# Performance work log

Hardware: AMD Instinct MI355X
Metric: run time of the kernel (lower is better)

## Reference

```python
import jax, jax.numpy as jnp
import numpy as np
from jax import lax

IN_PLANES = 512
GROWTH = 32
PLANES = 4 * GROWTH  # 128
EPS = 1e-5


def setup_inputs() -> dict:
    key = jax.random.key(0)
    ks = jax.random.split(key, 10)
    x = jax.random.normal(ks[0], (128, IN_PLANES, 32, 32), dtype=jnp.float32)
    # bn1 affine params (batch-stat BN, track_running_stats=False)
    gamma1 = jax.random.normal(ks[1], (IN_PLANES,), dtype=jnp.float32) * 0.1 + 1.0
    beta1 = jax.random.normal(ks[2], (IN_PLANES,), dtype=jnp.float32) * 0.1
    # convbn1: 1x1 conv weight + folded BN (running stats)
    w1 = jax.random.normal(ks[3], (PLANES, IN_PLANES, 1, 1), dtype=jnp.float32) * (1.0 / np.sqrt(IN_PLANES))
    gamma2 = jax.random.normal(ks[4], (PLANES,), dtype=jnp.float32) * 0.1 + 1.0
    beta2 = jax.random.normal(ks[5], (PLANES,), dtype=jnp.float32) * 0.1
    mean2 = jax.random.normal(ks[6], (PLANES,), dtype=jnp.float32) * 0.1
    var2 = jax.random.uniform(ks[7], (PLANES,), dtype=jnp.float32, minval=0.5, maxval=1.5)
    # conv2: 3x3 conv, padding 1, no bias
    w2 = jax.random.normal(ks[8], (GROWTH, PLANES, 3, 3), dtype=jnp.float32) * (1.0 / np.sqrt(9 * PLANES))
    return {"x": x, "gamma1": gamma1, "beta1": beta1, "w1": w1,
            "gamma2": gamma2, "beta2": beta2, "mean2": mean2, "var2": var2,
            "w2": w2}


def _bn(h, mean, var, gamma, beta):
    # channel-wise affine normalization, NCHW
    inv = lax.rsqrt(var + EPS)
    scale = (gamma * inv)[None, :, None, None]
    shift = (beta - mean * gamma * inv)[None, :, None, None]
    return h * scale + shift


def reference(x, gamma1, beta1, w1, gamma2, beta2, mean2, var2, w2):
    # bn1: batch statistics (track_running_stats=False)
    mu = jnp.mean(x, axis=(0, 2, 3))
    var = jnp.var(x, axis=(0, 2, 3))  # biased, as torch BN normalization
    h = _bn(x, mu, var, gamma1, beta1)
    h = jax.nn.relu(h)
    # convbn1: 1x1 conv then folded BN (running stats)
    h = lax.conv_general_dilated(h, w1, (1, 1), 'VALID',
                                 dimension_numbers=('NCHW', 'OIHW', 'NCHW'))
    h = _bn(h, mean2, var2, gamma2, beta2)
    h = jax.nn.relu(h)
    # conv2: 3x3, stride 1, pad 1, no bias
    out = lax.conv_general_dilated(h, w2, (1, 1), ((1, 1), (1, 1)),
                                   dimension_numbers=('NCHW', 'OIHW', 'NCHW'))
    # dense concat along channels
    return jnp.concatenate([x, out], axis=1)
```

## Files before the change

### kernel.cpp

```cpp
#include <hip/hip_runtime.h>

#define EPS 1e-5f

typedef __bf16 bf16x8 __attribute__((ext_vector_type(8)));
typedef __bf16 bf16x4 __attribute__((ext_vector_type(4)));
typedef unsigned short ushort8 __attribute__((ext_vector_type(8)));
typedef float f32x4 __attribute__((ext_vector_type(4)));

static __device__ __forceinline__ unsigned short f2bf(float f) {
  unsigned int u = __float_as_uint(f);
  u += 0x7fffu + ((u >> 16) & 1u);
  return (unsigned short)(u >> 16);
}


__global__ void prep_kernel(const float* __restrict__ w1,
                            const float* __restrict__ gamma2,
                            const float* __restrict__ beta2,
                            const float* __restrict__ mean2,
                            const float* __restrict__ var2,
                            const float* __restrict__ w2,
                            unsigned short* __restrict__ w1b,
                            unsigned short* __restrict__ w2b,
                            float* __restrict__ bias2) {
  int idx = blockIdx.x * 256 + threadIdx.x;
  if (idx < 128 * 512) {
    int oc = idx >> 9;
    float s2 = gamma2[oc] * rsqrtf(var2[oc] + EPS);
    w1b[idx] = f2bf(w1[idx] * s2);
  } else if (idx < 128 * 512 + 32 * 1152) {
    int i2 = idx - 128 * 512;
    int oc = i2 / 1152;
    int rem = i2 - oc * 1152;
    int tap = rem >> 7;
    int c = rem & 127;
    w2b[i2] = f2bf(w2[(oc * 128 + c) * 9 + tap]);
  } else if (idx < 128 * 512 + 32 * 1152 + 128) {
    int oc = idx - (128 * 512 + 32 * 1152);
    float s2 = gamma2[oc] * rsqrtf(var2[oc] + EPS);
    bias2[oc] = beta2[oc] - mean2[oc] * s2;
  }
}

__global__ void __launch_bounds__(256) stats_copy_kernel(
    const float* __restrict__ x, float* __restrict__ out,
    float* __restrict__ psum, float* __restrict__ psq) {
  const int c = blockIdx.x & 511;
  const int nq = blockIdx.x >> 9;
  const int t = threadIdx.x;
  float sum = 0.f, sq = 0.f;
  const f32x4* __restrict__ x4 = (const f32x4*)x;
  f32x4* out4 = (f32x4*)out;
#pragma unroll 4
  for (int i = 0; i < 16; ++i) {
    const int n = nq * 16 + i;
    f32x4 v = x4[(((size_t)n * 512 + c) << 8) + t];
    __builtin_nontemporal_store(v, &out4[(((size_t)n * 544 + c) << 8) + t]);
    sum += v[0] + v[1] + v[2] + v[3];
    sq += v[0] * v[0] + v[1] * v[1] + v[2] * v[2] + v[3] * v[3];
  }
  __shared__ float ls[2][4];
  for (int off = 32; off > 0; off >>= 1) {
    sum += __shfl_down(sum, off);
    sq += __shfl_down(sq, off);
  }
  const int w = t >> 6;
  if ((t & 63) == 0) { ls[0][w] = sum; ls[1][w] = sq; }
  __syncthreads();
  if (t == 0) {
    psum[c * 8 + nq] = ls[0][0] + ls[0][1] + ls[0][2] + ls[0][3];
    psq[c * 8 + nq] = ls[1][0] + ls[1][1] + ls[1][2] + ls[1][3];
  }
}

__global__ void reduce_kernel(const float* __restrict__ psum,
                              const float* __restrict__ psq,
                              const float* __restrict__ g1,
                              const float* __restrict__ be1,
                              float* __restrict__ s1, float* __restrict__ b1) {
  int c = blockIdx.x * 256 + threadIdx.x;
  if (c < 512) {
    float S = 0.f, Q = 0.f;
#pragma unroll
    for (int q = 0; q < 8; ++q) { S += psum[c * 8 + q]; Q += psq[c * 8 + q]; }
    float mean = S * (1.0f / 131072.0f);
    float var = Q * (1.0f / 131072.0f) - mean * mean;
    float s = g1[c] * rsqrtf(var + EPS);
    s1[c] = s;
    b1[c] = be1[c] - mean * s;
  }
}

__global__ void __launch_bounds__(256, 2) conv1_kernel(
    const float* __restrict__ x, const unsigned short* __restrict__ w1b,
    const float* __restrict__ s1, const float* __restrict__ b1,
    const float* __restrict__ bias2, unsigned short* __restrict__ h2) {
  const int t = threadIdx.x;
  const int lane = t & 63;
  const int wv = t >> 6;
  const int n = 127 - (blockIdx.x >> 2);
  const int p0w = (blockIdx.x & 3) * 256 + wv * 64;
  const int l15 = lane & 15;
  const int kb = lane >> 4;

  f32x4 acc[8][4];
#pragma unroll
  for (int m = 0; m < 8; ++m)
#pragma unroll
    for (int g = 0; g < 4; ++g) acc[m][g] = (f32x4){0.f, 0.f, 0.f, 0.f};

  const float* __restrict__ xn = x + (size_t)n * 512 * 1024;

  for (int c0 = 0; c0 < 512; c0 += 32) {
    const int cbase = c0 + kb * 8;
    float s1v[8], b1v[8];
#pragma unroll
    for (int j = 0; j < 8; ++j) {
      s1v[j] = s1[cbase + j];
      b1v[j] = b1[cbase + j];
    }
    bf16x8 bf[4];
#pragma unroll
    for (int g = 0; g < 4; ++g) {
      const int p = p0w + g * 16 + l15;
      bf16x8 tmp;
#pragma unroll
      for (int j = 0; j < 8; ++j) {
        float xv = xn[(size_t)(cbase + j) * 1024 + p];
        float a = fmaxf(fmaf(xv, s1v[j], b1v[j]), 0.f);
        tmp[j] = (__bf16)a;
      }
      bf[g] = tmp;
    }
#pragma unroll
    for (int m = 0; m < 8; ++m) {
      bf16x8 af = *(const bf16x8*)(w1b + (size_t)(m * 16 + l15) * 512 + cbase);
#pragma unroll
      for (int g = 0; g < 4; ++g)
        acc[m][g] = __builtin_amdgcn_mfma_f32_16x16x32_bf16(af, bf[g], acc[m][g], 0, 0, 0);
    }
  }

#pragma unroll
  for (int m = 0; m < 8; ++m) {
    const int ocb = m * 16 + kb * 4;
    float bz0 = bias2[ocb + 0], bz1 = bias2[ocb + 1];
    float bz2 = bias2[ocb + 2], bz3 = bias2[ocb + 3];
#pragma unroll
    for (int g = 0; g < 4; ++g) {
      const int p = p0w + g * 16 + l15;
      bf16x4 hv;
      hv[0] = (__bf16)fmaxf(acc[m][g][0] + bz0, 0.f);
      hv[1] = (__bf16)fmaxf(acc[m][g][1] + bz1, 0.f);
      hv[2] = (__bf16)fmaxf(acc[m][g][2] + bz2, 0.f);
      hv[3] = (__bf16)fmaxf(acc[m][g][3] + bz3, 0.f);
      *(bf16x4*)(h2 + ((size_t)n * 1024 + p) * 128 + ocb) = hv;
    }
  }
}

__global__ void __launch_bounds__(256) conv2_kernel(
    const unsigned short* __restrict__ h2, const unsigned short* __restrict__ w2b,
    float* __restrict__ out) {
  const int t = threadIdx.x;
  const int lane = t & 63;
  const int wv = t >> 6;
  const int n = blockIdx.x >> 2;
  const int pbase = (blockIdx.x & 3) * 256 + wv * 64;
  const int l15 = lane & 15;
  const int kb = lane >> 4;

  f32x4 acc[2][4];
#pragma unroll
  for (int m = 0; m < 2; ++m)
#pragma unroll
    for (int g = 0; g < 4; ++g) acc[m][g] = (f32x4){0.f, 0.f, 0.f, 0.f};

  const unsigned short* __restrict__ h2n = h2 + (size_t)n * 1024 * 128;

#pragma unroll
  for (int tap = 0; tap < 9; ++tap) {
    const int dy = tap / 3 - 1;
    const int dx = tap % 3 - 1;
#pragma unroll
    for (int c0 = 0; c0 < 128; c0 += 32) {
      const int cb = c0 + kb * 8;
      bf16x8 af[2];
#pragma unroll
      for (int m = 0; m < 2; ++m)
        af[m] = *(const bf16x8*)(w2b + (size_t)(m * 16 + l15) * 1152 + tap * 128 + cb);
#pragma unroll
      for (int g = 0; g < 4; ++g) {
        const int p = pbase + g * 16 + l15;
        const int y = (p >> 5) & 31;
        const int xx = p & 31;
        const int y2 = y + dy;
        const int x2 = xx + dx;
        bf16x8 bv = __builtin_bit_cast(bf16x8, (ushort8){0, 0, 0, 0, 0, 0, 0, 0});
        if (y2 >= 0 && y2 < 32 && x2 >= 0 && x2 < 32)
          bv = *(const bf16x8*)(h2n + ((size_t)(y2 * 32 + x2)) * 128 + cb);
#pragma unroll
        for (int m = 0; m < 2; ++m)
          acc[m][g] = __builtin_amdgcn_mfma_f32_16x16x32_bf16(af[m], bv, acc[m][g], 0, 0, 0);
      }
    }
  }

#pragma unroll
  for (int m = 0; m < 2; ++m) {
    const int oc = m * 16 + kb * 4;
#pragma unroll
    for (int g = 0; g < 4; ++g) {
      const int p = pbase + g * 16 + l15;
#pragma unroll
      for (int r = 0; r < 4; ++r)
        __builtin_nontemporal_store(
            acc[m][g][r], &out[((size_t)n * 544 + 512 + oc + r) * 1024 + p]);
    }
  }
}

extern "C" void kernel_launch(void* const* d_in, const int* in_sizes, int n_in,
                              void* d_out, int out_size, void* d_ws, size_t ws_size,
                              hipStream_t stream) {
  const float* x = (const float*)d_in[0];
  const float* gamma1 = (const float*)d_in[1];
  const float* beta1 = (const float*)d_in[2];
  const float* w1 = (const float*)d_in[3];
  const float* gamma2 = (const float*)d_in[4];
  const float* beta2 = (const float*)d_in[5];
  const float* mean2 = (const float*)d_in[6];
  const float* var2 = (const float*)d_in[7];
  const float* w2 = (const float*)d_in[8];
  float* out = (float*)d_out;

  char* ws = (char*)d_ws;
  unsigned short* h2 = (unsigned short*)ws;
  unsigned short* w1b = (unsigned short*)(ws + 33554432);
  unsigned short* w2b = (unsigned short*)(ws + 33685504);
  float* s1 = (float*)(ws + 33759232);
  float* b1 = (float*)(ws + 33761280);
  float* bias2 = (float*)(ws + 33763328);
  float* psum = (float*)(ws + 33763840);
  float* psq = (float*)(ws + 33780224);

  prep_kernel<<<401, 256, 0, stream>>>(w1, gamma2, beta2, mean2, var2, w2, w1b, w2b, bias2);
  stats_copy_kernel<<<4096, 256, 0, stream>>>(x, out, psum, psq);
  reduce_kernel<<<2, 256, 0, stream>>>(psum, psq, gamma1, beta1, s1, b1);
  conv1_kernel<<<512, 256, 0, stream>>>(x, w1b, s1, b1, bias2, h2);
  conv2_kernel<<<512, 256, 0, stream>>>(h2, w2b, out);
}
```

Baseline: 207.2 us.

## Stage bf16 copy of x in stats pass and merge prep/reduce kernels

The statistics/copy kernel now also writes a bf16 copy of x, and conv1 reads that copy instead of the fp32 input, halving the bytes it loads. Weight preparation is merged into the stats launch as extra blocks. The per-channel BN reduction is recomputed in each conv1 block into shared memory, which removes two launches. The cost is an extra 128 MB write and bf16 rounding of x before the batch-norm affine, a small accuracy change.

```diff
diff --git a/kernel.cpp b/kernel.cpp
--- a/kernel.cpp
+++ b/kernel.cpp
@@ -14,48 +14,50 @@
 }
 
 
-__global__ void prep_kernel(const float* __restrict__ w1,
-                            const float* __restrict__ gamma2,
-                            const float* __restrict__ beta2,
-                            const float* __restrict__ mean2,
-                            const float* __restrict__ var2,
-                            const float* __restrict__ w2,
-                            unsigned short* __restrict__ w1b,
-                            unsigned short* __restrict__ w2b,
-                            float* __restrict__ bias2) {
-  int idx = blockIdx.x * 256 + threadIdx.x;
-  if (idx < 128 * 512) {
-    int oc = idx >> 9;
-    float s2 = gamma2[oc] * rsqrtf(var2[oc] + EPS);
-    w1b[idx] = f2bf(w1[idx] * s2);
-  } else if (idx < 128 * 512 + 32 * 1152) {
-    int i2 = idx - 128 * 512;
-    int oc = i2 / 1152;
-    int rem = i2 - oc * 1152;
-    int tap = rem >> 7;
-    int c = rem & 127;
-    w2b[i2] = f2bf(w2[(oc * 128 + c) * 9 + tap]);
-  } else if (idx < 128 * 512 + 32 * 1152 + 128) {
-    int oc = idx - (128 * 512 + 32 * 1152);
-    float s2 = gamma2[oc] * rsqrtf(var2[oc] + EPS);
-    bias2[oc] = beta2[oc] - mean2[oc] * s2;
-  }
-}
-
-__global__ void __launch_bounds__(256) stats_copy_kernel(
+__global__ void __launch_bounds__(256) k1_kernel(
     const float* __restrict__ x, float* __restrict__ out,
-    float* __restrict__ psum, float* __restrict__ psq) {
+    unsigned short* __restrict__ xbf,
+    float* __restrict__ psum, float* __restrict__ psq,
+    const float* __restrict__ w1, const float* __restrict__ gamma2,
+    const float* __restrict__ beta2, const float* __restrict__ mean2,
+    const float* __restrict__ var2, const float* __restrict__ w2,
+    unsigned short* __restrict__ w1b, unsigned short* __restrict__ w2b,
+    float* __restrict__ bias2) {
+  const int t = threadIdx.x;
+  if (blockIdx.x >= 4096) {
+    int idx = (blockIdx.x - 4096) * 256 + t;
+    if (idx < 128 * 512) {
+      int oc = idx >> 9;
+      float s2 = gamma2[oc] * rsqrtf(var2[oc] + EPS);
+      w1b[idx] = f2bf(w1[idx] * s2);
+    } else if (idx < 128 * 512 + 32 * 1152) {
+      int i2 = idx - 128 * 512;
+      int oc = i2 / 1152;
+      int rem = i2 - oc * 1152;
+      int tap = rem >> 7;
+      int c = rem & 127;
+      w2b[i2] = f2bf(w2[(oc * 128 + c) * 9 + tap]);
+    } else if (idx < 128 * 512 + 32 * 1152 + 128) {
+      int oc = idx - (128 * 512 + 32 * 1152);
+      float s2 = gamma2[oc] * rsqrtf(var2[oc] + EPS);
+      bias2[oc] = beta2[oc] - mean2[oc] * s2;
+    }
+    return;
+  }
   const int c = blockIdx.x & 511;
   const int nq = blockIdx.x >> 9;
-  const int t = threadIdx.x;
   float sum = 0.f, sq = 0.f;
   const f32x4* __restrict__ x4 = (const f32x4*)x;
   f32x4* out4 = (f32x4*)out;
 #pragma unroll 4
   for (int i = 0; i < 16; ++i) {
     const int n = nq * 16 + i;
-    f32x4 v = x4[(((size_t)n * 512 + c) << 8) + t];
+    f32x4 v = __builtin_nontemporal_load(&x4[(((size_t)n * 512 + c) << 8) + t]);
     __builtin_nontemporal_store(v, &out4[(((size_t)n * 544 + c) << 8) + t]);
+    bf16x4 bv;
+    bv[0] = (__bf16)v[0]; bv[1] = (__bf16)v[1];
+    bv[2] = (__bf16)v[2]; bv[3] = (__bf16)v[3];
+    *(bf16x4*)(xbf + (((size_t)n * 512 + c) << 10) + t * 4) = bv;
     sum += v[0] + v[1] + v[2] + v[3];
     sq += v[0] * v[0] + v[1] * v[1] + v[2] * v[2] + v[3] * v[3];
   }
@@ -73,29 +75,25 @@
   }
 }
 
-__global__ void reduce_kernel(const float* __restrict__ psum,
-                              const float* __restrict__ psq,
-                              const float* __restrict__ g1,
-                              const float* __restrict__ be1,
-                              float* __restrict__ s1, float* __restrict__ b1) {
-  int c = blockIdx.x * 256 + threadIdx.x;
-  if (c < 512) {
+__global__ void __launch_bounds__(256, 2) conv1_kernel(
+    const unsigned short* __restrict__ xbf, const unsigned short* __restrict__ w1b,
+    const float* __restrict__ psum, const float* __restrict__ psq,
+    const float* __restrict__ g1, const float* __restrict__ be1,
+    const float* __restrict__ bias2, unsigned short* __restrict__ h2) {
+  const int t = threadIdx.x;
+  __shared__ float s1s[512], b1s[512];
+  for (int cc = t; cc < 512; cc += 256) {
     float S = 0.f, Q = 0.f;
 #pragma unroll
-    for (int q = 0; q < 8; ++q) { S += psum[c * 8 + q]; Q += psq[c * 8 + q]; }
+    for (int q = 0; q < 8; ++q) { S += psum[cc * 8 + q]; Q += psq[cc * 8 + q]; }
     float mean = S * (1.0f / 131072.0f);
     float var = Q * (1.0f / 131072.0f) - mean * mean;
-    float s = g1[c] * rsqrtf(var + EPS);
-    s1[c] = s;
-    b1[c] = be1[c] - mean * s;
-  }
-}
-
-__global__ void __launch_bounds__(256, 2) conv1_kernel(
-    const float* __restrict__ x, const unsigned short* __restrict__ w1b,
-    const float* __restrict__ s1, const float* __restrict__ b1,
-    const float* __restrict__ bias2, unsigned short* __restrict__ h2) {
-  const int t = threadIdx.x;
+    float s = g1[cc] * rsqrtf(var + EPS);
+    s1s[cc] = s;
+    b1s[cc] = be1[cc] - mean * s;
+  }
+  __syncthreads();
+
   const int lane = t & 63;
   const int wv = t >> 6;
   const int n = 127 - (blockIdx.x >> 2);
@@ -109,15 +107,15 @@
 #pragma unroll
     for (int g = 0; g < 4; ++g) acc[m][g] = (f32x4){0.f, 0.f, 0.f, 0.f};
 
-  const float* __restrict__ xn = x + (size_t)n * 512 * 1024;
+  const unsigned short* __restrict__ xn = xbf + (size_t)n * 512 * 1024;
 
   for (int c0 = 0; c0 < 512; c0 += 32) {
     const int cbase = c0 + kb * 8;
     float s1v[8], b1v[8];
 #pragma unroll
     for (int j = 0; j < 8; ++j) {
-      s1v[j] = s1[cbase + j];
-      b1v[j] = b1[cbase + j];
+      s1v[j] = s1s[cbase + j];
+      b1v[j] = b1s[cbase + j];
     }
     bf16x8 bf[4];
 #pragma unroll
@@ -126,7 +124,7 @@
       bf16x8 tmp;
 #pragma unroll
       for (int j = 0; j < 8; ++j) {
-        float xv = xn[(size_t)(cbase + j) * 1024 + p];
+        float xv = (float)*(const __bf16*)(xn + ((size_t)(cbase + j) << 10) + p);
         float a = fmaxf(fmaf(xv, s1v[j], b1v[j]), 0.f);
         tmp[j] = (__bf16)a;
       }
@@ -236,17 +234,16 @@
 
   char* ws = (char*)d_ws;
   unsigned short* h2 = (unsigned short*)ws;
-  unsigned short* w1b = (unsigned short*)(ws + 33554432);
-  unsigned short* w2b = (unsigned short*)(ws + 33685504);
-  float* s1 = (float*)(ws + 33759232);
-  float* b1 = (float*)(ws + 33761280);
-  float* bias2 = (float*)(ws + 33763328);
-  float* psum = (float*)(ws + 33763840);
-  float* psq = (float*)(ws + 33780224);
-
-  prep_kernel<<<401, 256, 0, stream>>>(w1, gamma2, beta2, mean2, var2, w2, w1b, w2b, bias2);
-  stats_copy_kernel<<<4096, 256, 0, stream>>>(x, out, psum, psq);
-  reduce_kernel<<<2, 256, 0, stream>>>(psum, psq, gamma1, beta1, s1, b1);
-  conv1_kernel<<<512, 256, 0, stream>>>(x, w1b, s1, b1, bias2, h2);
+  unsigned short* xbf = (unsigned short*)(ws + 33554432);
+  unsigned short* w1b = (unsigned short*)(ws + 167772160);
+  unsigned short* w2b = (unsigned short*)(ws + 167903232);
+  float* bias2 = (float*)(ws + 167976960);
+  float* psum = (float*)(ws + 167977472);
+  float* psq = (float*)(ws + 167993856);
+
+  k1_kernel<<<4512, 256, 0, stream>>>(x, out, xbf, psum, psq,
+                                      w1, gamma2, beta2, mean2, var2, w2,
+                                      w1b, w2b, bias2);
+  conv1_kernel<<<512, 256, 0, stream>>>(xbf, w1b, psum, psq, gamma1, beta1, bias2, h2);
   conv2_kernel<<<512, 256, 0, stream>>>(h2, w2b, out);
 }
```

Result: faster. 200.4 us (-3.3%).

## Merge weight prep into stats kernel and stage conv1 input through LDS tile

Applied to the files above, without the earlier changes.

The weight-prep kernel is folded into the stats/copy kernel as extra blocks, which removes one launch. Conv1 now loads x with coalesced float4 reads along pixels, applies BN1+ReLU, and writes bf16 to a padded shared-memory tile. MFMA B operands are then gathered from that tile, and the next channel chunk is prefetched into registers. BN1 scale and shift are cached in LDS, and the stats loop unroll is raised to 8. The cost is two barriers per channel chunk, extra LDS use, and scalar bf16 LDS reads that may limit occupancy.

```diff
diff --git a/kernel.cpp b/kernel.cpp
--- a/kernel.cpp
+++ b/kernel.cpp
@@ -14,44 +14,41 @@
 }
 
 
-__global__ void prep_kernel(const float* __restrict__ w1,
-                            const float* __restrict__ gamma2,
-                            const float* __restrict__ beta2,
-                            const float* __restrict__ mean2,
-                            const float* __restrict__ var2,
-                            const float* __restrict__ w2,
-                            unsigned short* __restrict__ w1b,
-                            unsigned short* __restrict__ w2b,
-                            float* __restrict__ bias2) {
-  int idx = blockIdx.x * 256 + threadIdx.x;
-  if (idx < 128 * 512) {
-    int oc = idx >> 9;
-    float s2 = gamma2[oc] * rsqrtf(var2[oc] + EPS);
-    w1b[idx] = f2bf(w1[idx] * s2);
-  } else if (idx < 128 * 512 + 32 * 1152) {
-    int i2 = idx - 128 * 512;
-    int oc = i2 / 1152;
-    int rem = i2 - oc * 1152;
-    int tap = rem >> 7;
-    int c = rem & 127;
-    w2b[i2] = f2bf(w2[(oc * 128 + c) * 9 + tap]);
-  } else if (idx < 128 * 512 + 32 * 1152 + 128) {
-    int oc = idx - (128 * 512 + 32 * 1152);
-    float s2 = gamma2[oc] * rsqrtf(var2[oc] + EPS);
-    bias2[oc] = beta2[oc] - mean2[oc] * s2;
-  }
-}
-
-__global__ void __launch_bounds__(256) stats_copy_kernel(
+__global__ void __launch_bounds__(256) k1_kernel(
     const float* __restrict__ x, float* __restrict__ out,
-    float* __restrict__ psum, float* __restrict__ psq) {
+    float* __restrict__ psum, float* __restrict__ psq,
+    const float* __restrict__ w1, const float* __restrict__ gamma2,
+    const float* __restrict__ beta2, const float* __restrict__ mean2,
+    const float* __restrict__ var2, const float* __restrict__ w2,
+    unsigned short* __restrict__ w1b, unsigned short* __restrict__ w2b,
+    float* __restrict__ bias2) {
+  const int t = threadIdx.x;
+  if (blockIdx.x >= 4096) {
+    int idx = (blockIdx.x - 4096) * 256 + t;
+    if (idx < 128 * 512) {
+      int oc = idx >> 9;
+      float s2 = gamma2[oc] * rsqrtf(var2[oc] + EPS);
+      w1b[idx] = f2bf(w1[idx] * s2);
+    } else if (idx < 128 * 512 + 32 * 1152) {
+      int i2 = idx - 128 * 512;
+      int oc = i2 / 1152;
+      int rem = i2 - oc * 1152;
+      int tap = rem >> 7;
+      int c = rem & 127;
+      w2b[i2] = f2bf(w2[(oc * 128 + c) * 9 + tap]);
+    } else if (idx < 128 * 512 + 32 * 1152 + 128) {
+      int oc = idx - (128 * 512 + 32 * 1152);
+      float s2 = gamma2[oc] * rsqrtf(var2[oc] + EPS);
+      bias2[oc] = beta2[oc] - mean2[oc] * s2;
+    }
+    return;
+  }
   const int c = blockIdx.x & 511;
   const int nq = blockIdx.x >> 9;
-  const int t = threadIdx.x;
   float sum = 0.f, sq = 0.f;
   const f32x4* __restrict__ x4 = (const f32x4*)x;
   f32x4* out4 = (f32x4*)out;
-#pragma unroll 4
+#pragma unroll 8
   for (int i = 0; i < 16; ++i) {
     const int n = nq * 16 + i;
     f32x4 v = x4[(((size_t)n * 512 + c) << 8) + t];
@@ -96,10 +93,18 @@
     const float* __restrict__ s1, const float* __restrict__ b1,
     const float* __restrict__ bias2, unsigned short* __restrict__ h2) {
   const int t = threadIdx.x;
+  __shared__ float s1s[512], b1s[512];
+  __shared__ __align__(16) unsigned short tile[32 * 260];
+  for (int cc = t; cc < 512; cc += 256) {
+    s1s[cc] = s1[cc];
+    b1s[cc] = b1[cc];
+  }
+  __syncthreads();
+
   const int lane = t & 63;
   const int wv = t >> 6;
   const int n = 127 - (blockIdx.x >> 2);
-  const int p0w = (blockIdx.x & 3) * 256 + wv * 64;
+  const int q = blockIdx.x & 3;
   const int l15 = lane & 15;
   const int kb = lane >> 4;
 
@@ -109,36 +114,50 @@
 #pragma unroll
     for (int g = 0; g < 4; ++g) acc[m][g] = (f32x4){0.f, 0.f, 0.f, 0.f};
 
-  const float* __restrict__ xn = x + (size_t)n * 512 * 1024;
-
-  for (int c0 = 0; c0 < 512; c0 += 32) {
-    const int cbase = c0 + kb * 8;
-    float s1v[8], b1v[8];
-#pragma unroll
-    for (int j = 0; j < 8; ++j) {
-      s1v[j] = s1[cbase + j];
-      b1v[j] = b1[cbase + j];
-    }
+  const f32x4* __restrict__ xq = (const f32x4*)(x + (size_t)n * 524288 + q * 256);
+
+  f32x4 v[8];
+#pragma unroll
+  for (int i = 0; i < 8; ++i)
+    v[i] = xq[(size_t)(wv * 8 + i) * 256 + lane];
+
+  for (int k = 0; k < 16; ++k) {
+    const int c0 = k * 32;
+#pragma unroll
+    for (int i = 0; i < 8; ++i) {
+      const int c = c0 + wv * 8 + i;
+      const float s = s1s[c], b = b1s[c];
+      bf16x4 bv;
+      bv[0] = (__bf16)fmaxf(fmaf(v[i][0], s, b), 0.f);
+      bv[1] = (__bf16)fmaxf(fmaf(v[i][1], s, b), 0.f);
+      bv[2] = (__bf16)fmaxf(fmaf(v[i][2], s, b), 0.f);
+      bv[3] = (__bf16)fmaxf(fmaf(v[i][3], s, b), 0.f);
+      *(bf16x4*)&tile[(size_t)(wv * 8 + i) * 260 + 4 * lane] = bv;
+    }
+    if (k < 15) {
+#pragma unroll
+      for (int i = 0; i < 8; ++i)
+        v[i] = xq[(size_t)(c0 + 32 + wv * 8 + i) * 256 + lane];
+    }
+    __syncthreads();
     bf16x8 bf[4];
 #pragma unroll
     for (int g = 0; g < 4; ++g) {
-      const int p = p0w + g * 16 + l15;
+      const int pl = wv * 64 + g * 16 + l15;
       bf16x8 tmp;
 #pragma unroll
-      for (int j = 0; j < 8; ++j) {
-        float xv = xn[(size_t)(cbase + j) * 1024 + p];
-        float a = fmaxf(fmaf(xv, s1v[j], b1v[j]), 0.f);
-        tmp[j] = (__bf16)a;
-      }
+      for (int j = 0; j < 8; ++j)
+        tmp[j] = __builtin_bit_cast(__bf16, tile[(kb * 8 + j) * 260 + pl]);
       bf[g] = tmp;
     }
 #pragma unroll
     for (int m = 0; m < 8; ++m) {
-      bf16x8 af = *(const bf16x8*)(w1b + (size_t)(m * 16 + l15) * 512 + cbase);
+      bf16x8 af = *(const bf16x8*)(w1b + (size_t)(m * 16 + l15) * 512 + c0 + kb * 8);
 #pragma unroll
       for (int g = 0; g < 4; ++g)
         acc[m][g] = __builtin_amdgcn_mfma_f32_16x16x32_bf16(af, bf[g], acc[m][g], 0, 0, 0);
     }
+    __syncthreads();
   }
 
 #pragma unroll
@@ -148,7 +167,7 @@
     float bz2 = bias2[ocb + 2], bz3 = bias2[ocb + 3];
 #pragma unroll
     for (int g = 0; g < 4; ++g) {
-      const int p = p0w + g * 16 + l15;
+      const int p = q * 256 + wv * 64 + g * 16 + l15;
       bf16x4 hv;
       hv[0] = (__bf16)fmaxf(acc[m][g][0] + bz0, 0.f);
       hv[1] = (__bf16)fmaxf(acc[m][g][1] + bz1, 0.f);
@@ -238,14 +257,15 @@
   unsigned short* h2 = (unsigned short*)ws;
   unsigned short* w1b = (unsigned short*)(ws + 33554432);
   unsigned short* w2b = (unsigned short*)(ws + 33685504);
-  float* s1 = (float*)(ws + 33759232);
-  float* b1 = (float*)(ws + 33761280);
-  float* bias2 = (float*)(ws + 33763328);
+  float* bias2 = (float*)(ws + 33759232);
+  float* s1 = (float*)(ws + 33759744);
+  float* b1 = (float*)(ws + 33761792);
   float* psum = (float*)(ws + 33763840);
   float* psq = (float*)(ws + 33780224);
 
-  prep_kernel<<<401, 256, 0, stream>>>(w1, gamma2, beta2, mean2, var2, w2, w1b, w2b, bias2);
-  stats_copy_kernel<<<4096, 256, 0, stream>>>(x, out, psum, psq);
+  k1_kernel<<<4497, 256, 0, stream>>>(x, out, psum, psq,
+                                      w1, gamma2, beta2, mean2, var2, w2,
+                                      w1b, w2b, bias2);
   reduce_kernel<<<2, 256, 0, stream>>>(psum, psq, gamma1, beta1, s1, b1);
   conv1_kernel<<<512, 256, 0, stream>>>(x, w1b, s1, b1, bias2, h2);
   conv2_kernel<<<512, 256, 0, stream>>>(h2, w2b, out);
```

Result: faster. 199.3 us (-3.8%).
